# Kernel optimization log

Hardware: AMD Instinct MI355X
Metric: run time of the kernel (lower is better)

The kernel has to match this reference:

```python
import jax, jax.numpy as jnp
import numpy as np

E = 16          # total experts (two halves of 8)
E_HALF = 8
K = 2           # top-k per token
CAP_FACTOR = 2  # expert capacity factor over the average load


def setup_inputs() -> dict:
    key = jax.random.key(0)
    ks = jax.random.split(key, 6)
    N, D, F = 16384, 1024, 1024  # tokens, d_model, d_ff (repo uses d_ff == d_model)
    s = 0.02
    return {
        "moe_inp": jax.random.normal(ks[0], (N, D), jnp.float32),
        "gate_w": jax.random.normal(ks[1], (D, E), jnp.float32) * s,   # gate Linear(d_model, 16)
        "gate_b": jnp.zeros((E,), jnp.float32),
        "route_w": jax.random.normal(ks[2], (D, 1), jnp.float32) * s,  # self.weights Linear(d_model, 1)
        "route_b": jnp.zeros((1,), jnp.float32),
        "W1": jax.random.normal(ks[3], (E, D, F), jnp.float32) * s,    # htoh4 per expert
        "b1": jnp.zeros((E, F), jnp.float32),
        "W2": jax.random.normal(ks[4], (E, F, D), jnp.float32) * s,    # h4toh per expert
        "b2": jnp.zeros((E, D), jnp.float32),
    }


def reference(moe_inp, gate_w, gate_b, route_w, route_b, W1, b1, W2, b2):
    N, D = moe_inp.shape
    # --- gate: logits over 16 experts; half 1 -> experts [0,8), half 2 -> experts [8,16)
    logits = moe_inp @ gate_w + gate_b                       # [N, E]
    val1, idx1 = jax.lax.top_k(logits[:, :E_HALF], K)        # [N, K]
    score1 = jax.nn.softmax(val1, axis=-1)
    val2, idx2 = jax.lax.top_k(logits[:, E_HALF:], K)
    score2 = jax.nn.softmax(val2, axis=-1)
    idx2 = idx2 + E_HALF                                     # shift into second expert range (gate_top_k_idx_2 + 8)
    # --- hard binary split of tokens via sigmoid(Linear(d,1)) > 0.5
    group1 = jax.nn.sigmoid(moe_inp @ route_w + route_b) > 0.5   # [N, 1]
    idx = jnp.where(group1, idx1, idx2)                      # [N, K] combined routing
    score = jnp.where(group1, score1, score2)                # [N, K]
    # --- dispatch: flatten (token, slot) pairs, capacity-bucket per expert
    T = N * K
    C = CAP_FACTOR * T // E                                  # expert capacity
    flat_idx = idx.reshape(-1)                               # [T]
    flat_x = jnp.repeat(moe_inp, K, axis=0)                  # [T, D]
    onehot = jax.nn.one_hot(flat_idx, E, dtype=jnp.int32)    # [T, E]
    pos_in_e = (jnp.cumsum(onehot, axis=0) * onehot).sum(axis=1) - 1  # [T] slot within expert
    valid = pos_in_e < C
    safe_pos = jnp.where(valid, pos_in_e, 0)
    buf = jnp.zeros((E, C, D), moe_inp.dtype).at[flat_idx, safe_pos].add(
        jnp.where(valid[:, None], flat_x, 0.0))              # [E, C, D] contiguous per-expert inputs
    # --- grouped expert FFN: relu(x W1 + b1) W2 + b2 (dropout = identity in eval)
    h = jax.nn.relu(jnp.einsum('ecd,edf->ecf', buf, W1) + b1[:, None, :])
    y = jnp.einsum('ecf,efd->ecd', h, W2) + b2[:, None, :]   # [E, C, D]
    # --- gather back and combine with gate scores
    y_flat = jnp.where(valid[:, None], y[flat_idx, safe_pos], 0.0)   # [T, D]
    out = (y_flat.reshape(N, K, D) * score[..., None]).sum(axis=1)   # [N, D]
    return out
```

## Files before the change

kernel.cpp:

```cpp
#include <hip/hip_runtime.h>
#include <hip/hip_bf16.h>
#include <stdint.h>

#define N_TOK 16384
#define DMODEL 1024
#define EXP 16
#define CAP 4096
#define TT 32768

typedef __bf16 bf16x8 __attribute__((ext_vector_type(8)));
typedef __bf16 bf16x4 __attribute__((ext_vector_type(4)));
typedef float  f32x4  __attribute__((ext_vector_type(4)));

__device__ __forceinline__ void gl_lds16(const void* g, void* s) {
  __builtin_amdgcn_global_load_lds(
      (__attribute__((address_space(1))) void*)(void*)g,
      (__attribute__((address_space(3))) void*)s, 16, 0, 0);
}

__device__ __forceinline__ float bfbits2f(unsigned short u) {
  return __uint_as_float(((unsigned)u) << 16);
}

__global__ __launch_bounds__(256) void convw_kernel(const float* __restrict__ W1,
                                                    const float* __restrict__ W2,
                                                    __bf16* __restrict__ W1bt,
                                                    __bf16* __restrict__ W2bt) {
  __shared__ float tile[64][65];
  int b = blockIdx.x;
  int tx = b & 15;
  int ty = (b >> 4) & 15;
  int e  = (b >> 8) & 15;
  int which = (b >> 12) & 1;
  const float* src = (which ? W2 : W1) + (size_t)e * DMODEL * DMODEL;
  __bf16*      dst = (which ? W2bt : W1bt) + (size_t)e * DMODEL * DMODEL;
  int t = threadIdx.x;
  int r = t >> 2;
  int cs = (t & 3) * 16;
  int r0 = ty * 64, c0 = tx * 64;
  #pragma unroll
  for (int i = 0; i < 16; i += 4) {
    float4 v = *(const float4*)(src + (size_t)(r0 + r) * DMODEL + c0 + cs + i);
    tile[r][cs + i + 0] = v.x; tile[r][cs + i + 1] = v.y;
    tile[r][cs + i + 2] = v.z; tile[r][cs + i + 3] = v.w;
  }
  __syncthreads();
  bf16x8 o1, o2;
  #pragma unroll
  for (int i = 0; i < 8; i++) o1[i] = (__bf16)tile[cs + i][r];
  #pragma unroll
  for (int i = 0; i < 8; i++) o2[i] = (__bf16)tile[cs + 8 + i][r];
  *(bf16x8*)(dst + (size_t)(c0 + r) * DMODEL + r0 + cs)     = o1;
  *(bf16x8*)(dst + (size_t)(c0 + r) * DMODEL + r0 + cs + 8) = o2;
}

__global__ __launch_bounds__(256) void gate_kernel(const float* __restrict__ x,
                                                   const float* __restrict__ gw,
                                                   const float* __restrict__ gb,
                                                   const float* __restrict__ rw,
                                                   const float* __restrict__ rb,
                                                   int* __restrict__ idxo,
                                                   float* __restrict__ sco,
                                                   __bf16* __restrict__ Xb) {
  __shared__ float gws[512 * 17];
  __shared__ float rws[512];
  int tid = threadIdx.x;
  int w = tid >> 6, lane = tid & 63;
  int n = blockIdx.x * 4 + w;
  const float* xr = x + (size_t)n * DMODEL;
  __bf16* xbr = Xb + (size_t)n * DMODEL;

  float acc[17];
  #pragma unroll
  for (int j = 0; j < 17; j++) acc[j] = 0.f;

  for (int c = 0; c < 2; c++) {
    int c0 = c * 512;
    __syncthreads();
    for (int i = tid; i < 512 * 16; i += 256)
      gws[(i >> 4) * 17 + (i & 15)] = gw[c0 * 16 + i];
    for (int i = tid; i < 512; i += 256)
      rws[i] = rw[c0 + i];
    __syncthreads();

    float xv[8];
    #pragma unroll
    for (int u = 0; u < 8; u++) xv[u] = xr[c0 + u * 64 + lane];
    #pragma unroll
    for (int u = 0; u < 8; u++) xbr[c0 + u * 64 + lane] = (__bf16)xv[u];
    #pragma unroll
    for (int u = 0; u < 8; u++) {
      int dl = u * 64 + lane;
      const float* g = &gws[dl * 17];
      #pragma unroll
      for (int j = 0; j < 16; j++) acc[j] += xv[u] * g[j];
      acc[16] += xv[u] * rws[dl];
    }
  }

  #pragma unroll
  for (int o = 1; o < 64; o <<= 1) {
    #pragma unroll
    for (int j = 0; j < 17; j++) acc[j] += __shfl_xor(acc[j], o);
  }
  if (lane == 0) {
    float rv = acc[16] + rb[0];
    bool g1 = rv > 0.f;
    float c[8];
    #pragma unroll
    for (int j = 0; j < 8; j++)
      c[j] = (g1 ? acc[j] + gb[j] : acc[8 + j] + gb[8 + j]);
    int i1 = 0; float v1 = c[0];
    #pragma unroll
    for (int j = 1; j < 8; j++) { if (c[j] > v1) { v1 = c[j]; i1 = j; } }
    int i2 = -1; float v2 = -3.4e38f;
    #pragma unroll
    for (int j = 0; j < 8; j++) { if (j != i1 && c[j] > v2) { v2 = c[j]; i2 = j; } }
    float e2 = expf(v2 - v1);
    float den = 1.f + e2;
    int base = g1 ? 0 : 8;
    idxo[2 * n] = base + i1; idxo[2 * n + 1] = base + i2;
    sco[2 * n] = 1.f / den;  sco[2 * n + 1] = e2 / den;
  }
}

__global__ __launch_bounds__(1024) void scan_kernel(const int* __restrict__ idx,
                                                    float* __restrict__ sco,
                                                    int* __restrict__ rowlist,
                                                    int* __restrict__ cnt,
                                                    int* __restrict__ off) {
  __shared__ int hist[16 * 1024];
  int tid = threadIdx.x;
  #pragma unroll
  for (int e = 0; e < 16; e++) hist[e * 1024 + tid] = 0;
  __syncthreads();
  int base = tid * 32;
  for (int i = 0; i < 32; i++) {
    int e = idx[base + i];
    hist[e * 1024 + tid]++;
  }
  __syncthreads();
  int w = tid >> 6, lane = tid & 63;
  {
    int e = w;
    int running = 0;
    for (int cch = 0; cch < 16; cch++) {
      int v = hist[e * 1024 + cch * 64 + lane];
      int orig = v;
      #pragma unroll
      for (int o = 1; o < 64; o <<= 1) {
        int nv = __shfl_up(v, o);
        if (lane >= o) v += nv;
      }
      hist[e * 1024 + cch * 64 + lane] = running + v - orig;
      running += __shfl(v, 63);
    }
    if (lane == 0) cnt[e] = running;
  }
  __syncthreads();
  if (tid == 0) {
    int o = 0;
    for (int e = 0; e < 16; e++) {
      int c = cnt[e]; if (c > CAP) c = CAP;
      off[e] = o; cnt[e] = c; o += c;
    }
  }
  __syncthreads();
  for (int i = 0; i < 32; i++) {
    int t = base + i;
    int e = idx[t];
    int r = hist[e * 1024 + tid]++;
    if (r < CAP) rowlist[e * CAP + r] = t;
    else sco[t] = 0.f;
  }
}

#define GBM 256
#define GBN 256
#define GBK 64
#define NKT (DMODEL / GBK)

__global__ __launch_bounds__(512) void moe_gemm(const __bf16* __restrict__ A,
                                                const __bf16* __restrict__ Bt,
                                                const float* __restrict__ bias,
                                                __bf16* __restrict__ out,
                                                const int* __restrict__ rowlist,
                                                const int* __restrict__ cnt,
                                                const int* __restrict__ off,
                                                int mode) {
  __shared__ char lds[131072];
  int bx = blockIdx.x;
  int em = (bx & 7) * 32 + (bx >> 3);
  int e  = em >> 4;
  int m0 = (em & 15) * GBM;
  int ce = cnt[e];
  if (m0 >= ce) return;
  int n0 = blockIdx.y * GBN;
  int oe = off[e];
  int tid = threadIdx.x;

  const __bf16* aP[4];
  const __bf16* bP[4];
  #pragma unroll
  for (int j = 0; j < 4; j++) {
    int lin = j * 512 + tid;
    int r = lin >> 3;
    int g = lin & 7;
    int rr = m0 + r; if (rr > ce - 1) rr = ce - 1;
    size_t arow;
    if (mode == 0) arow = (size_t)(rowlist[e * CAP + rr] >> 1);
    else           arow = (size_t)(oe + rr);
    aP[j] = A + arow * DMODEL + g * 8;
    bP[j] = Bt + (size_t)e * DMODEL * DMODEL + (size_t)(n0 + r) * DMODEL + g * 8;
  }

  int w = tid >> 6, lane = tid & 63;
  int wr = (w >> 2) * 128;
  int wc = (w & 3) * 64;
  int fr = lane & 15, fg = lane >> 4;

  f32x4 acc[8][4];
  #pragma unroll
  for (int mi = 0; mi < 8; mi++)
    #pragma unroll
    for (int ni = 0; ni < 4; ni++)
      #pragma unroll
      for (int l = 0; l < 4; l++) acc[mi][ni][l] = 0.f;

  #pragma unroll
  for (int j = 0; j < 4; j++) {
    gl_lds16(aP[j], lds + (size_t)(j * 512 + tid) * 16);
    gl_lds16(bP[j], lds + 65536 + (size_t)(j * 512 + tid) * 16);
  }
  __syncthreads();

  int cur = 0;
  for (int t = 0; t < NKT; t++) {
    if (t < NKT - 1) {
      int k0 = (t + 1) * GBK;
      char* Ad = lds + (cur ^ 1) * 32768;
      char* Bd = lds + 65536 + (cur ^ 1) * 32768;
      #pragma unroll
      for (int j = 0; j < 4; j++) {
        gl_lds16(aP[j] + k0, Ad + (size_t)(j * 512 + tid) * 16);
        gl_lds16(bP[j] + k0, Bd + (size_t)(j * 512 + tid) * 16);
      }
    }
    char* As = lds + cur * 32768;
    char* Bs = lds + 65536 + cur * 32768;
    #pragma unroll
    for (int kk = 0; kk < 2; kk++) {
      bf16x8 af[8], bfr[4];
      #pragma unroll
      for (int mi = 0; mi < 8; mi++)
        af[mi] = *(const bf16x8*)(As + (size_t)(wr + mi * 16 + fr) * 128 + kk * 64 + fg * 16);
      #pragma unroll
      for (int ni = 0; ni < 4; ni++)
        bfr[ni] = *(const bf16x8*)(Bs + (size_t)(wc + ni * 16 + fr) * 128 + kk * 64 + fg * 16);
      #pragma unroll
      for (int mi = 0; mi < 8; mi++)
        #pragma unroll
        for (int ni = 0; ni < 4; ni++)
          acc[mi][ni] = __builtin_amdgcn_mfma_f32_16x16x32_bf16(af[mi], bfr[ni], acc[mi][ni], 0, 0, 0);
    }
    __syncthreads();
    cur ^= 1;
  }

  float bcol[4];
  #pragma unroll
  for (int ni = 0; ni < 4; ni++)
    bcol[ni] = bias[(size_t)e * DMODEL + n0 + wc + ni * 16 + fr];
  #pragma unroll
  for (int mi = 0; mi < 8; mi++) {
    #pragma unroll
    for (int r = 0; r < 4; r++) {
      int grow = m0 + wr + mi * 16 + fg * 4 + r;
      if (grow >= ce) continue;
      size_t orow = (mode == 0) ? (size_t)(oe + grow)
                                : (size_t)rowlist[e * CAP + grow];
      __bf16* op = out + orow * DMODEL + n0 + wc + fr;
      #pragma unroll
      for (int ni = 0; ni < 4; ni++) {
        float v = acc[mi][ni][r] + bcol[ni];
        if (mode == 0) v = fmaxf(v, 0.f);
        op[ni * 16] = (__bf16)v;
      }
    }
  }
}

__global__ __launch_bounds__(256) void combine_kernel(const __bf16* __restrict__ y,
                                                      const float* __restrict__ sco,
                                                      float* __restrict__ out) {
  int n = blockIdx.x;
  int d = threadIdx.x * 4;
  float s0 = sco[2 * n], s1 = sco[2 * n + 1];
  ushort4 a = *(const ushort4*)((const unsigned short*)(y + (size_t)(2 * n) * DMODEL + d));
  ushort4 b = *(const ushort4*)((const unsigned short*)(y + (size_t)(2 * n + 1) * DMODEL + d));
  float4 o;
  o.x = s0 * bfbits2f(a.x) + s1 * bfbits2f(b.x);
  o.y = s0 * bfbits2f(a.y) + s1 * bfbits2f(b.y);
  o.z = s0 * bfbits2f(a.z) + s1 * bfbits2f(b.z);
  o.w = s0 * bfbits2f(a.w) + s1 * bfbits2f(b.w);
  *(float4*)(out + (size_t)n * DMODEL + d) = o;
}

extern "C" void kernel_launch(void* const* d_in, const int* in_sizes, int n_in,
                              void* d_out, int out_size, void* d_ws, size_t ws_size,
                              hipStream_t stream) {
  const float* moe = (const float*)d_in[0];
  const float* gw  = (const float*)d_in[1];
  const float* gb  = (const float*)d_in[2];
  const float* rw  = (const float*)d_in[3];
  const float* rb  = (const float*)d_in[4];
  const float* W1  = (const float*)d_in[5];
  const float* b1  = (const float*)d_in[6];
  const float* W2  = (const float*)d_in[7];
  const float* b2  = (const float*)d_in[8];
  float* out = (float*)d_out;

  char* p = (char*)d_ws;
  __bf16* Xb   = (__bf16*)p; p += (size_t)N_TOK * DMODEL * 2;
  __bf16* W1bt = (__bf16*)p; p += (size_t)EXP * DMODEL * DMODEL * 2;
  __bf16* W2bt = (__bf16*)p; p += (size_t)EXP * DMODEL * DMODEL * 2;
  __bf16* hbuf = (__bf16*)p; p += (size_t)TT * DMODEL * 2;
  __bf16* ybuf = (__bf16*)p; p += (size_t)TT * DMODEL * 2;
  int*   idxb   = (int*)p;   p += (size_t)TT * 4;
  float* scoreb = (float*)p; p += (size_t)TT * 4;
  int*   rowlist = (int*)p;  p += (size_t)EXP * CAP * 4;
  int*   cntb    = (int*)p;  p += 64;
  int*   offb    = (int*)p;  p += 64;

  convw_kernel<<<dim3(8192), dim3(256), 0, stream>>>(W1, W2, W1bt, W2bt);
  gate_kernel<<<dim3(4096), dim3(256), 0, stream>>>(moe, gw, gb, rw, rb, idxb, scoreb, Xb);
  scan_kernel<<<dim3(1), dim3(1024), 0, stream>>>(idxb, scoreb, rowlist, cntb, offb);
  moe_gemm<<<dim3(256, 4), dim3(512), 0, stream>>>(Xb, W1bt, b1, hbuf, rowlist, cntb, offb, 0);
  moe_gemm<<<dim3(256, 4), dim3(512), 0, stream>>>(hbuf, W2bt, b2, ybuf, rowlist, cntb, offb, 1);
  combine_kernel<<<dim3(16384), dim3(256), 0, stream>>>(ybuf, scoreb, out);
}
```

Before: 428.6 us.

## Restructure grouped GEMM mainloop into quarter-staged ping-pong with swizzled LDS

Rewrites the grouped expert GEMM main loop so each K-step is split into four MFMA quadrants. Global-to-LDS loads for A and B halves are interleaved between the quadrants with explicit barriers, vmcnt waits and s_setprio, so memory traffic overlaps compute. An XOR swizzle on the 16-byte chunk index is added to cut LDS bank conflicts on fragment reads. Warp tile ownership is remapped to match the new half-buffer layout. The staging is hand-counted and relies on exact vmcnt values and buffer reuse ordering, so a miscount would corrupt data.

Result: faster. 411.0 us (-4.1%).

```diff
diff --git a/kernel.cpp b/kernel.cpp
--- a/kernel.cpp
+++ b/kernel.cpp
@@ -21,6 +21,9 @@
 __device__ __forceinline__ float bfbits2f(unsigned short u) {
   return __uint_as_float(((unsigned)u) << 16);
 }
+
+#define FENCE asm volatile("" ::: "memory")
+#define BAR() do { FENCE; __builtin_amdgcn_s_barrier(); FENCE; } while (0)
 
 __global__ __launch_bounds__(256) void convw_kernel(const float* __restrict__ W1,
                                                     const float* __restrict__ W2,
@@ -199,26 +202,34 @@
   int oe = off[e];
   int tid = threadIdx.x;
 
-  const __bf16* aP[4];
-  const __bf16* bP[4];
-  #pragma unroll
-  for (int j = 0; j < 4; j++) {
-    int lin = j * 512 + tid;
-    int r = lin >> 3;
-    int g = lin & 7;
-    int rr = m0 + r; if (rr > ce - 1) rr = ce - 1;
-    size_t arow;
-    if (mode == 0) arow = (size_t)(rowlist[e * CAP + rr] >> 1);
-    else           arow = (size_t)(oe + rr);
-    aP[j] = A + arow * DMODEL + g * 8;
-    bP[j] = Bt + (size_t)e * DMODEL * DMODEL + (size_t)(n0 + r) * DMODEL + g * 8;
-  }
+  const __bf16* aP[2][2];
+  const __bf16* bP[2][2];
+  #pragma unroll
+  for (int h = 0; h < 2; h++)
+    #pragma unroll
+    for (int j = 0; j < 2; j++) {
+      int lin = j * 512 + tid;
+      int srow = lin >> 3;
+      int gsrc = (lin & 7) ^ (srow & 7);
+      int rr = m0 + h * 128 + srow; if (rr > ce - 1) rr = ce - 1;
+      size_t arow;
+      if (mode == 0) arow = (size_t)(rowlist[e * CAP + rr] >> 1);
+      else           arow = (size_t)(oe + rr);
+      aP[h][j] = A + arow * DMODEL + gsrc * 8;
+      bP[h][j] = Bt + (size_t)e * DMODEL * DMODEL + (size_t)(n0 + h * 128 + srow) * DMODEL + gsrc * 8;
+    }
 
   int w = tid >> 6, lane = tid & 63;
-  int wr = (w >> 2) * 128;
-  int wc = (w & 3) * 64;
+  int ah = w >> 2;
+  int bh = (w & 3) >> 1;
+  int bl = (w & 1) * 64;
   int fr = lane & 15, fg = lane >> 4;
 
+  int aRd = ah * 16384 + fr * 128;
+  int bRd = 65536 + bh * 16384 + (bl + fr) * 128;
+  int gk0 = ((fg)     ^ (fr & 7)) * 16;
+  int gk1 = ((4 | fg) ^ (fr & 7)) * 16;
+
   f32x4 acc[8][4];
   #pragma unroll
   for (int mi = 0; mi < 8; mi++)
@@ -227,46 +238,103 @@
       #pragma unroll
       for (int l = 0; l < 4; l++) acc[mi][ni][l] = 0.f;
 
-  #pragma unroll
-  for (int j = 0; j < 4; j++) {
-    gl_lds16(aP[j], lds + (size_t)(j * 512 + tid) * 16);
-    gl_lds16(bP[j], lds + 65536 + (size_t)(j * 512 + tid) * 16);
-  }
-  __syncthreads();
-
-  int cur = 0;
-  for (int t = 0; t < NKT; t++) {
-    if (t < NKT - 1) {
-      int k0 = (t + 1) * GBK;
-      char* Ad = lds + (cur ^ 1) * 32768;
-      char* Bd = lds + 65536 + (cur ^ 1) * 32768;
-      #pragma unroll
-      for (int j = 0; j < 4; j++) {
-        gl_lds16(aP[j] + k0, Ad + (size_t)(j * 512 + tid) * 16);
-        gl_lds16(bP[j] + k0, Bd + (size_t)(j * 512 + tid) * 16);
-      }
-    }
-    char* As = lds + cur * 32768;
-    char* Bs = lds + 65536 + cur * 32768;
-    #pragma unroll
-    for (int kk = 0; kk < 2; kk++) {
-      bf16x8 af[8], bfr[4];
-      #pragma unroll
-      for (int mi = 0; mi < 8; mi++)
-        af[mi] = *(const bf16x8*)(As + (size_t)(wr + mi * 16 + fr) * 128 + kk * 64 + fg * 16);
-      #pragma unroll
-      for (int ni = 0; ni < 4; ni++)
-        bfr[ni] = *(const bf16x8*)(Bs + (size_t)(wc + ni * 16 + fr) * 128 + kk * 64 + fg * 16);
-      #pragma unroll
-      for (int mi = 0; mi < 8; mi++)
+  auto stA = [&](int s, int h) {
+    char* dst = lds + (s & 1) * 32768 + h * 16384;
+    gl_lds16(aP[h][0] + s * 64, dst + (size_t)tid * 16);
+    gl_lds16(aP[h][1] + s * 64, dst + (size_t)(512 + tid) * 16);
+  };
+  auto stB = [&](int s, int h) {
+    char* dst = lds + 65536 + (s & 1) * 32768 + h * 16384;
+    gl_lds16(bP[h][0] + s * 64, dst + (size_t)tid * 16);
+    gl_lds16(bP[h][1] + s * 64, dst + (size_t)(512 + tid) * 16);
+  };
+
+  stA(0, 0); stA(0, 1); stB(0, 0); stB(0, 1);
+  stA(1, 0); stA(1, 1); stB(1, 0); stB(1, 1);
+  asm volatile("s_waitcnt vmcnt(8)" ::: "memory");
+  BAR();
+
+  bf16x8 afA[4][2], bq0[2][2], bq1[2][2];
+  for (int t = 0; t < NKT; ++t) {
+    const char* Ab = lds + (t & 1) * 32768 + aRd;
+    const char* Bb = lds + (t & 1) * 32768 + bRd;
+
+    #pragma unroll
+    for (int mi = 0; mi < 4; mi++) {
+      afA[mi][0] = *(const bf16x8*)(Ab + mi * 2048 + gk0);
+      afA[mi][1] = *(const bf16x8*)(Ab + mi * 2048 + gk1);
+    }
+    #pragma unroll
+    for (int ni = 0; ni < 2; ni++) {
+      bq0[ni][0] = *(const bf16x8*)(Bb + ni * 2048 + gk0);
+      bq0[ni][1] = *(const bf16x8*)(Bb + ni * 2048 + gk1);
+    }
+    if (t >= 1 && t <= 14) stA(t + 1, 0);
+    BAR();
+    __builtin_amdgcn_s_setprio(1);
+    #pragma unroll
+    for (int kk = 0; kk < 2; kk++)
+      #pragma unroll
+      for (int mi = 0; mi < 4; mi++)
         #pragma unroll
-        for (int ni = 0; ni < 4; ni++)
-          acc[mi][ni] = __builtin_amdgcn_mfma_f32_16x16x32_bf16(af[mi], bfr[ni], acc[mi][ni], 0, 0, 0);
-    }
-    __syncthreads();
-    cur ^= 1;
-  }
-
+        for (int ni = 0; ni < 2; ni++)
+          acc[mi][ni] = __builtin_amdgcn_mfma_f32_16x16x32_bf16(afA[mi][kk], bq0[ni][kk], acc[mi][ni], 0, 0, 0);
+    __builtin_amdgcn_s_setprio(0);
+    BAR();
+
+    #pragma unroll
+    for (int ni = 0; ni < 2; ni++) {
+      bq1[ni][0] = *(const bf16x8*)(Bb + (2 + ni) * 2048 + gk0);
+      bq1[ni][1] = *(const bf16x8*)(Bb + (2 + ni) * 2048 + gk1);
+    }
+    if (t >= 1 && t <= 14) stA(t + 1, 1);
+    BAR();
+    __builtin_amdgcn_s_setprio(1);
+    #pragma unroll
+    for (int kk = 0; kk < 2; kk++)
+      #pragma unroll
+      for (int mi = 0; mi < 4; mi++)
+        #pragma unroll
+        for (int ni = 0; ni < 2; ni++)
+          acc[mi][2 + ni] = __builtin_amdgcn_mfma_f32_16x16x32_bf16(afA[mi][kk], bq1[ni][kk], acc[mi][2 + ni], 0, 0, 0);
+    __builtin_amdgcn_s_setprio(0);
+    BAR();
+
+    #pragma unroll
+    for (int mi = 0; mi < 4; mi++) {
+      afA[mi][0] = *(const bf16x8*)(Ab + (4 + mi) * 2048 + gk0);
+      afA[mi][1] = *(const bf16x8*)(Ab + (4 + mi) * 2048 + gk1);
+    }
+    if (t <= 13) stB(t + 2, 0);
+    BAR();
+    __builtin_amdgcn_s_setprio(1);
+    #pragma unroll
+    for (int kk = 0; kk < 2; kk++)
+      #pragma unroll
+      for (int mi = 0; mi < 4; mi++)
+        #pragma unroll
+        for (int ni = 0; ni < 2; ni++)
+          acc[4 + mi][2 + ni] = __builtin_amdgcn_mfma_f32_16x16x32_bf16(afA[mi][kk], bq1[ni][kk], acc[4 + mi][2 + ni], 0, 0, 0);
+    __builtin_amdgcn_s_setprio(0);
+    BAR();
+
+    if (t <= 13) stB(t + 2, 1);
+    BAR();
+    __builtin_amdgcn_s_setprio(1);
+    #pragma unroll
+    for (int kk = 0; kk < 2; kk++)
+      #pragma unroll
+      for (int mi = 0; mi < 4; mi++)
+        #pragma unroll
+        for (int ni = 0; ni < 2; ni++)
+          acc[4 + mi][ni] = __builtin_amdgcn_mfma_f32_16x16x32_bf16(afA[mi][kk], bq0[ni][kk], acc[4 + mi][ni], 0, 0, 0);
+    __builtin_amdgcn_s_setprio(0);
+    if (t <= 13)      asm volatile("s_waitcnt vmcnt(4)" ::: "memory");
+    else if (t == 14) asm volatile("s_waitcnt vmcnt(0)" ::: "memory");
+    BAR();
+  }
+
+  int wr = ah * 128, wc = (w & 3) * 64;
   float bcol[4];
   #pragma unroll
   for (int ni = 0; ni < 4; ni++)
```
